# Kernel optimization log

Measured on AMD Instinct MI355X. Metric: run time of the kernel, lower is better.

The kernel has to match this reference:

```python
import jax, jax.numpy as jnp
import numpy as np

S, B, D, N, DH = 2048, 2, 1024, 16, 64  # seq, batch, d_model, n_head, d_head
LN_EPS = 1e-5


def setup_inputs() -> dict:
    key = jax.random.key(0)
    ks = jax.random.split(key, 8)
    h = jax.random.normal(ks[0], (S, B, D), dtype=jnp.float32)
    Wq = jax.random.normal(ks[1], (D, N * DH), dtype=jnp.float32) * 0.02
    Wkv = jax.random.normal(ks[2], (D, 2 * N * DH), dtype=jnp.float32) * 0.02
    Wo = jax.random.normal(ks[3], (N * DH, D), dtype=jnp.float32) * 0.02
    ln_gamma = jnp.ones((D,), dtype=jnp.float32)
    ln_beta = jnp.zeros((D,), dtype=jnp.float32)
    # persistent compressive-memory state from a previous segment
    memory = jax.random.normal(ks[4], (B, N, DH, DH), dtype=jnp.float32)
    # normalization is a sum of (elu(k)+1) over ~S positions -> strictly positive, O(S)
    mem_norm = jax.random.uniform(ks[5], (B, 1, N, DH), dtype=jnp.float32) * S + 1.0
    gate_beta = jnp.ones((1,), dtype=jnp.float32) * 0.01  # beta_eps
    return {"h": h, "Wq": Wq, "Wkv": Wkv, "Wo": Wo, "ln_gamma": ln_gamma,
            "ln_beta": ln_beta, "memory": memory, "mem_norm": mem_norm,
            "gate_beta": gate_beta}


def reference(h, Wq, Wkv, Wo, ln_gamma, ln_beta, memory, mem_norm, gate_beta):
    scale = 1.0 / np.sqrt(DH).astype(np.float32)
    # projections (pre_lnorm=False, mems=None -> c == h)
    q = (h @ Wq).reshape(S, B, N, DH)
    k, v = jnp.split(h @ Wkv, 2, axis=-1)
    k = k.reshape(S, B, N, DH)
    v = v.reshape(S, B, N, DH)
    # local quadratic attention
    score = jnp.einsum('ibnd,jbnd->ijbn', q, k) * scale  # [S,S,B,N]
    prob = jax.nn.softmax(score, axis=1)
    attn_vec = jnp.einsum('ijbn,jbnd->ibnd', prob, v).reshape(S, B, N * DH)
    # memory retrieval (NOTE: source swaps K/V in the _update_memory call;
    # it is done under no_grad -> stop_gradient here)
    cached_Q = jax.nn.elu(q.swapaxes(0, 1)) + 1.0          # [B,S,N,DH]
    num = jnp.einsum('bsnk,bnkv->bsnv', cached_Q, memory)   # [B,S,N,DH]
    den = jnp.einsum('bsnk,bvnk->bsnv', cached_Q, mem_norm)  # [B,S,N,1]
    content_A = jax.lax.stop_gradient(num / den)            # [B,S,N,DH]
    # gated injection
    g = jax.nn.sigmoid(gate_beta)                           # [1]
    inj = g * content_A.swapaxes(0, 1).reshape(S, B, N * DH) + (1.0 - g) * attn_vec
    attn_out = inj @ Wo
    # post layernorm residual
    y = h + attn_out
    mu = jnp.mean(y, axis=-1, keepdims=True)
    var = jnp.mean((y - mu) ** 2, axis=-1, keepdims=True)
    return (y - mu) / jnp.sqrt(var + LN_EPS) * ln_gamma + ln_beta
```

## Files before the change

kernel.cpp:

```cpp
#include <hip/hip_runtime.h>


typedef unsigned short ushort_t;
typedef unsigned int uint32;

typedef __bf16 bf16x8 __attribute__((ext_vector_type(8)));
typedef float f32x4 __attribute__((ext_vector_type(4)));
typedef float f32x16 __attribute__((ext_vector_type(16)));
typedef unsigned short u16x8 __attribute__((ext_vector_type(8)));
typedef unsigned short u16x4 __attribute__((ext_vector_type(4)));
typedef unsigned int u32x4 __attribute__((ext_vector_type(4)));

typedef const __attribute__((address_space(1))) void gvoid_t;
typedef __attribute__((address_space(3))) void lvoid_t;

#define S_LEN 2048
#define BATCH 2
#define NHEAD 16

__device__ __forceinline__ ushort_t f2bf(float x) {
  union { float f; unsigned u; } c; c.f = x;
  unsigned r = (c.u + 0x7FFFu + ((c.u >> 16) & 1u)) >> 16;
  return (ushort_t)r;
}
__device__ __forceinline__ float bf2f(ushort_t v) {
  union { unsigned u; float f; } c; c.u = ((unsigned)v) << 16;
  return c.f;
}

__global__ __launch_bounds__(256) void k_cvt_h(const float* __restrict__ src,
                                               ushort_t* __restrict__ dst, int n4) {
  int idx = blockIdx.x * 256 + threadIdx.x;
  if (idx >= n4) return;
  float4 v = ((const float4*)src)[idx];
  u16x4 o; o[0] = f2bf(v.x); o[1] = f2bf(v.y); o[2] = f2bf(v.z); o[3] = f2bf(v.w);
  ((u16x4*)dst)[idx] = o;
}

__global__ __launch_bounds__(256) void k_cvt_wT(const float* __restrict__ W,
                                                ushort_t* __restrict__ WT, int K, int N) {
  __shared__ float tile[32][33];
  const int n0 = blockIdx.x * 32, k0 = blockIdx.y * 32;
  const int tx = threadIdx.x & 31, ty = threadIdx.x >> 5;
#pragma unroll
  for (int r = 0; r < 32; r += 8)
    tile[ty + r][tx] = W[(size_t)(k0 + ty + r) * N + n0 + tx];
  __syncthreads();
#pragma unroll
  for (int r = 0; r < 32; r += 8)
    WT[(size_t)(n0 + ty + r) * K + k0 + tx] = f2bf(tile[tx][ty + r]);
}

template <int OUT_BF16>
__global__ __launch_bounds__(256) void k_gemm_bt(const ushort_t* __restrict__ A,
                                                 const ushort_t* __restrict__ B,
                                                 void* __restrict__ Cv, int M, int N, int K,
                                                 int nbx) {
  __shared__ __attribute__((aligned(16))) ushort_t As[128 * 32];
  __shared__ __attribute__((aligned(16))) ushort_t Bs[128 * 32];
  const int per = gridDim.x >> 3;
  const int fl = (blockIdx.x & 7) * per + (blockIdx.x >> 3);
  const int m0 = (fl / nbx) * 128, n0 = (fl % nbx) * 128;
  const int tid = threadIdx.x, w = tid >> 6, lane = tid & 63;
  const int wm = (w >> 1) * 64, wn = (w & 1) * 64;
  const int l15 = lane & 15, l4 = lane >> 4;
  f32x4 acc[4][4];
#pragma unroll
  for (int i = 0; i < 4; ++i)
#pragma unroll
    for (int j = 0; j < 4; ++j)
#pragma unroll
      for (int r = 0; r < 4; ++r) acc[i][j][r] = 0.f;

  for (int k0 = 0; k0 < K; k0 += 32) {
    __syncthreads();
#pragma unroll
    for (int r = 0; r < 2; ++r) {
      int c = r * 256 + w * 64 + lane;
      const ushort_t* ga = A + (size_t)(m0 + (c >> 2)) * K + k0 + (c & 3) * 8;
      const ushort_t* gb = B + (size_t)(n0 + (c >> 2)) * K + k0 + (c & 3) * 8;
      __builtin_amdgcn_global_load_lds((gvoid_t*)ga, (lvoid_t*)(As + (r * 256 + w * 64) * 8), 16, 0, 0);
      __builtin_amdgcn_global_load_lds((gvoid_t*)gb, (lvoid_t*)(Bs + (r * 256 + w * 64) * 8), 16, 0, 0);
    }
    __syncthreads();
    bf16x8 af[4], bfr[4];
#pragma unroll
    for (int i = 0; i < 4; ++i) af[i] = *(const bf16x8*)&As[(wm + i * 16 + l15) * 32 + l4 * 8];
#pragma unroll
    for (int j = 0; j < 4; ++j) bfr[j] = *(const bf16x8*)&Bs[(wn + j * 16 + l15) * 32 + l4 * 8];
#pragma unroll
    for (int i = 0; i < 4; ++i)
#pragma unroll
      for (int j = 0; j < 4; ++j)
        acc[i][j] = __builtin_amdgcn_mfma_f32_16x16x32_bf16(af[i], bfr[j], acc[i][j], 0, 0, 0);
  }
#pragma unroll
  for (int i = 0; i < 4; ++i)
#pragma unroll
    for (int j = 0; j < 4; ++j)
#pragma unroll
      for (int r = 0; r < 4; ++r) {
        int row = m0 + wm + i * 16 + l4 * 4 + r;
        int col = n0 + wn + j * 16 + l15;
        if (OUT_BF16)
          ((ushort_t*)Cv)[(size_t)row * N + col] = f2bf(acc[i][j][r]);
        else
          ((float*)Cv)[(size_t)row * N + col] = acc[i][j][r];
      }
}

__global__ __launch_bounds__(256) void k_gemm64(const ushort_t* __restrict__ A,
                                                const ushort_t* __restrict__ B,
                                                float* __restrict__ C, int M, int N, int K,
                                                int nbx) {
  __shared__ __attribute__((aligned(16))) ushort_t As[64 * 32];
  __shared__ __attribute__((aligned(16))) ushort_t Bs[128 * 32];
  const int per = gridDim.x >> 3;
  const int fl = (blockIdx.x & 7) * per + (blockIdx.x >> 3);
  const int m0 = (fl / nbx) * 64, n0 = (fl % nbx) * 128;
  const int tid = threadIdx.x, w = tid >> 6, lane = tid & 63;
  const int wn = w * 32;
  const int l15 = lane & 15, l4 = lane >> 4;
  f32x4 acc[4][2];
#pragma unroll
  for (int i = 0; i < 4; ++i)
#pragma unroll
    for (int j = 0; j < 2; ++j)
#pragma unroll
      for (int r = 0; r < 4; ++r) acc[i][j][r] = 0.f;

  for (int k0 = 0; k0 < K; k0 += 32) {
    __syncthreads();
    {
      int c = w * 64 + lane;
      const ushort_t* ga = A + (size_t)(m0 + (c >> 2)) * K + k0 + (c & 3) * 8;
      __builtin_amdgcn_global_load_lds((gvoid_t*)ga, (lvoid_t*)(As + w * 512), 16, 0, 0);
#pragma unroll
      for (int r = 0; r < 2; ++r) {
        int c2 = r * 256 + w * 64 + lane;
        const ushort_t* gb = B + (size_t)(n0 + (c2 >> 2)) * K + k0 + (c2 & 3) * 8;
        __builtin_amdgcn_global_load_lds((gvoid_t*)gb, (lvoid_t*)(Bs + r * 2048 + w * 512), 16, 0, 0);
      }
    }
    __syncthreads();
    bf16x8 af[4], bfr[2];
#pragma unroll
    for (int i = 0; i < 4; ++i) af[i] = *(const bf16x8*)&As[(i * 16 + l15) * 32 + l4 * 8];
#pragma unroll
    for (int j = 0; j < 2; ++j) bfr[j] = *(const bf16x8*)&Bs[(wn + j * 16 + l15) * 32 + l4 * 8];
#pragma unroll
    for (int i = 0; i < 4; ++i)
#pragma unroll
      for (int j = 0; j < 2; ++j)
        acc[i][j] = __builtin_amdgcn_mfma_f32_16x16x32_bf16(af[i], bfr[j], acc[i][j], 0, 0, 0);
  }
#pragma unroll
  for (int i = 0; i < 4; ++i)
#pragma unroll
    for (int j = 0; j < 2; ++j)
#pragma unroll
      for (int r = 0; r < 4; ++r)
        C[(size_t)(m0 + i * 16 + l4 * 4 + r) * N + n0 + wn + j * 16 + l15] = acc[i][j][r];
}

__global__ __launch_bounds__(256) void k_vt(const ushort_t* __restrict__ qkv,
                                            ushort_t* __restrict__ vt) {
  __shared__ uint32 tile[64 * 65];
  const int jt = blockIdx.x, bn = blockIdx.y, b = bn & 1, n = bn >> 1;
  const int tid = threadIdx.x;
  const int j0 = jt * 64;
#pragma unroll
  for (int rr = 0; rr < 2; ++rr) {
    int lin = rr * 2048 + tid * 8;
    int j = lin >> 6, d0 = lin & 63;
    u16x8 v = *(const u16x8*)(qkv + (size_t)(j0 + j) * 6144 + b * 3072 + 2048 + n * 64 + d0);
#pragma unroll
    for (int e = 0; e < 8; ++e) tile[j * 65 + d0 + e] = v[e];
  }
  __syncthreads();
#pragma unroll
  for (int rr = 0; rr < 2; ++rr) {
    int lin = rr * 2048 + tid * 8;
    int d = lin >> 6, jj = lin & 63;
    u16x8 o;
#pragma unroll
    for (int e = 0; e < 8; ++e) o[e] = (ushort_t)tile[(jj + e) * 65 + d];
    *(u16x8*)(vt + ((size_t)bn * 64 + d) * 2048 + j0 + jj) = o;
  }
}

__device__ __forceinline__ void stage_k(const ushort_t* __restrict__ qkv, ushort_t* kw,
                                        int j0, int b, int n, int w, int lane) {
#pragma unroll
  for (int r = 0; r < 2; ++r) {
    int jb_ = w * 16 + r * 8;
    int jb8 = w * 2 + r;
    const ushort_t* ksrc = qkv + (size_t)(j0 + jb_ + (lane >> 3)) * 6144 + b * 3072 + n * 64 + 1024
                           + ((((lane & 7) ^ (lane >> 3) ^ jb8) & 7) << 3);
    __builtin_amdgcn_global_load_lds((gvoid_t*)ksrc, (lvoid_t*)(kw + jb_ * 64), 16, 0, 0);
  }
}
__device__ __forceinline__ void stage_vt(const ushort_t* __restrict__ vt, ushort_t* vw,
                                         int j0, int bn, int w, int lane) {
#pragma unroll
  for (int r = 0; r < 2; ++r) {
    int db_ = w * 16 + r * 8;
    int jb8 = w * 2 + r;
    const ushort_t* vsrc = vt + ((size_t)bn * 64 + db_ + (lane >> 3)) * 2048 + j0
                           + ((((lane & 7) ^ (lane >> 3) ^ jb8) & 7) << 3);
    __builtin_amdgcn_global_load_lds((gvoid_t*)vsrc, (lvoid_t*)(vw + db_ * 64), 16, 0, 0);
  }
}

__global__ __launch_bounds__(256) void k_attn(const ushort_t* __restrict__ qkv,
                                              const ushort_t* __restrict__ vt,
                                              const float* __restrict__ mem,
                                              const float* __restrict__ mnorm,
                                              const float* __restrict__ gbeta,
                                              ushort_t* __restrict__ inj) {
  __shared__ __attribute__((aligned(16))) ushort_t Ks[2][4096];
  __shared__ __attribute__((aligned(16))) ushort_t VTs[2][4096];
  const int bn = blockIdx.y, b = bn & 1, n = bn >> 1;
  const int tid = threadIdx.x, w = tid >> 6, lane = tid & 63;
  const int l31 = lane & 31, h = lane >> 5;
  const int qrow = blockIdx.x * 128 + w * 32 + l31;
  const size_t qoff = (size_t)qrow * 6144 + b * 3072 + n * 64;
  const float CEXP = 0.18033688011113723f;
  bf16x8 qf[4];
#pragma unroll
  for (int ks = 0; ks < 4; ++ks) {
    u16x8 qv = *(const u16x8*)(qkv + qoff + ks * 16 + h * 8);
    union { u16x8 u; bf16x8 v; } cu;
#pragma unroll
    for (int e = 0; e < 8; ++e) cu.u[e] = f2bf(bf2f(qv[e]) * CEXP);
    qf[ks] = cu.v;
  }
  const int fA = (l31 & 7) ^ (l31 >> 3);
  const int fB = fA ^ 4;
  union { u16x8 u; bf16x8 v; } ones;
#pragma unroll
  for (int e = 0; e < 8; ++e) ones.u[e] = 0x3F80;

  stage_k(qkv, Ks[0], 0, b, n, w, lane);
  stage_vt(vt, VTs[0], 0, bn, w, lane);
  __syncthreads();

  f32x16 oacc[2], lacc;
#pragma unroll
  for (int r = 0; r < 16; ++r) { oacc[0][r] = 0.f; oacc[1][r] = 0.f; lacc[r] = 0.f; }

  for (int t = 0; t < 32; ++t) {
    const ushort_t* Kb = Ks[t & 1];
    const ushort_t* Vb = VTs[t & 1];
    if (t < 31) {
      stage_k(qkv, Ks[(t + 1) & 1], (t + 1) * 64, b, n, w, lane);
      stage_vt(vt, VTs[(t + 1) & 1], (t + 1) * 64, bn, w, lane);
    }
    f32x16 sv[2];
#pragma unroll
    for (int r = 0; r < 16; ++r) { sv[0][r] = 0.f; sv[1][r] = 0.f; }
    __builtin_amdgcn_s_setprio(1);
#pragma unroll
    for (int jb = 0; jb < 2; ++jb) {
      const int rb = (jb * 32 + l31) * 64;
      const int fj = jb ? fB : fA;
#pragma unroll
      for (int ks = 0; ks < 4; ++ks) {
        bf16x8 kf = *(const bf16x8*)&Kb[rb + ((((ks << 1) | h) ^ fj) << 3)];
        sv[jb] = __builtin_amdgcn_mfma_f32_32x32x16_bf16(kf, qf[ks], sv[jb], 0, 0, 0);
      }
    }
    __builtin_amdgcn_s_setprio(0);
#pragma unroll
    for (int jb = 0; jb < 2; ++jb)
#pragma unroll
      for (int r = 0; r < 16; ++r)
        sv[jb][r] = __builtin_amdgcn_exp2f(sv[jb][r]);
#pragma unroll
    for (int ks = 0; ks < 4; ++ks) {
      const int jb = ks >> 1, q0 = (ks & 1) * 2;
      uint32 X0, X1, Y0, Y1;
      asm volatile("v_cvt_pk_bf16_f32 %0, %1, %2" : "=v"(X0) : "v"(sv[jb][q0 * 4 + 0]), "v"(sv[jb][q0 * 4 + 1]));
      asm volatile("v_cvt_pk_bf16_f32 %0, %1, %2" : "=v"(X1) : "v"(sv[jb][q0 * 4 + 2]), "v"(sv[jb][q0 * 4 + 3]));
      asm volatile("v_cvt_pk_bf16_f32 %0, %1, %2" : "=v"(Y0) : "v"(sv[jb][(q0 + 1) * 4 + 0]), "v"(sv[jb][(q0 + 1) * 4 + 1]));
      asm volatile("v_cvt_pk_bf16_f32 %0, %1, %2" : "=v"(Y1) : "v"(sv[jb][(q0 + 1) * 4 + 2]), "v"(sv[jb][(q0 + 1) * 4 + 3]));
      asm volatile("v_permlane32_swap_b32 %0, %1" : "+v"(X0), "+v"(Y0));
      asm volatile("v_permlane32_swap_b32 %0, %1" : "+v"(X1), "+v"(Y1));
      union { u32x4 u; bf16x8 v; } pf;
      pf.u[0] = X0; pf.u[1] = X1; pf.u[2] = Y0; pf.u[3] = Y1;
      const int c = (ks << 1) | h;
      bf16x8 vf0 = *(const bf16x8*)&Vb[l31 * 64 + ((c ^ fA) << 3)];
      bf16x8 vf1 = *(const bf16x8*)&Vb[(32 + l31) * 64 + ((c ^ fB) << 3)];
      __builtin_amdgcn_s_setprio(1);
      oacc[0] = __builtin_amdgcn_mfma_f32_32x32x16_bf16(vf0, pf.v, oacc[0], 0, 0, 0);
      oacc[1] = __builtin_amdgcn_mfma_f32_32x32x16_bf16(vf1, pf.v, oacc[1], 0, 0, 0);
      lacc = __builtin_amdgcn_mfma_f32_32x32x16_bf16(ones.v, pf.v, lacc, 0, 0, 0);
      __builtin_amdgcn_s_setprio(0);
    }
    if (t < 31) __syncthreads();
  }
  const float l_run = lacc[0];

  float den = 0.f;
  bf16x8 cqf[4];
  const float* nrm = mnorm + (size_t)(b * NHEAD + n) * 64;
#pragma unroll
  for (int ks = 0; ks < 4; ++ks) {
    u16x8 qv = *(const u16x8*)(qkv + qoff + ks * 16 + h * 8);
    union { u16x8 u; bf16x8 v; } cu;
#pragma unroll
    for (int e = 0; e < 8; ++e) {
      float x = bf2f(qv[e]);
      float c = (x > 0.f) ? (x + 1.f) : __builtin_amdgcn_exp2f(x * 1.4426950408889634f);
      cu.u[e] = f2bf(c);
      den += c * nrm[ks * 16 + h * 8 + e];
    }
    cqf[ks] = cu.v;
  }
  den += __shfl_xor(den, 32);

  const float* mb = mem + (size_t)(b * NHEAD + n) * 4096;
  f32x16 accv[2];
#pragma unroll
  for (int r = 0; r < 16; ++r) { accv[0][r] = 0.f; accv[1][r] = 0.f; }
#pragma unroll
  for (int db = 0; db < 2; ++db)
#pragma unroll
    for (int ks = 0; ks < 4; ++ks) {
      union { u16x8 u; bf16x8 v; } af;
#pragma unroll
      for (int e = 0; e < 8; ++e)
        af.u[e] = f2bf(mb[(size_t)(ks * 16 + h * 8 + e) * 64 + db * 32 + l31]);
      accv[db] = __builtin_amdgcn_mfma_f32_32x32x16_bf16(af.v, cqf[ks], accv[db], 0, 0, 0);
    }

  float g = 1.f / (1.f + expf(-gbeta[0]));
  float rden = 1.f / den, invl = 1.f / l_run;
  ushort_t* op = inj + (size_t)qrow * 2048 + b * 1024 + n * 64;
#pragma unroll
  for (int db = 0; db < 2; ++db)
#pragma unroll
    for (int qq = 0; qq < 4; ++qq) {
      u16x4 st;
#pragma unroll
      for (int m = 0; m < 4; ++m) {
        float content = accv[db][qq * 4 + m] * rden;
        float av = oacc[db][qq * 4 + m] * invl;
        st[m] = f2bf(g * content + (1.f - g) * av);
      }
      *(u16x4*)(op + db * 32 + qq * 8 + h * 4) = st;
    }
}

__global__ __launch_bounds__(256) void k_ln(const float* __restrict__ h,
                                            const float* __restrict__ ao,
                                            const float* __restrict__ gam,
                                            const float* __restrict__ bet,
                                            float* __restrict__ out) {
  const int m = blockIdx.x, t = threadIdx.x;
  const int lane = t & 63, w = t >> 6;
  __shared__ float redS[4], redQ[4];
  const size_t base = (size_t)m * 1024;
  float4 hv = ((const float4*)(h + base))[t];
  float4 avv = ((const float4*)(ao + base))[t];
  float y0 = hv.x + avv.x, y1 = hv.y + avv.y, y2 = hv.z + avv.z, y3 = hv.w + avv.w;
  float s = y0 + y1 + y2 + y3;
  float sq = y0 * y0 + y1 * y1 + y2 * y2 + y3 * y3;
#pragma unroll
  for (int mk = 32; mk >= 1; mk >>= 1) { s += __shfl_xor(s, mk); sq += __shfl_xor(sq, mk); }
  if (lane == 0) { redS[w] = s; redQ[w] = sq; }
  __syncthreads();
  float Ssum = redS[0] + redS[1] + redS[2] + redS[3];
  float Qsum = redQ[0] + redQ[1] + redQ[2] + redQ[3];
  float mu = Ssum * (1.f / 1024.f);
  float var = Qsum * (1.f / 1024.f) - mu * mu;
  float rstd = rsqrtf(var + 1e-5f);
  float4 g = ((const float4*)gam)[t];
  float4 bt = ((const float4*)bet)[t];
  float4 o;
  o.x = (y0 - mu) * rstd * g.x + bt.x;
  o.y = (y1 - mu) * rstd * g.y + bt.y;
  o.z = (y2 - mu) * rstd * g.z + bt.z;
  o.w = (y3 - mu) * rstd * g.w + bt.w;
  ((float4*)(out + base))[t] = o;
}

extern "C" void kernel_launch(void* const* d_in, const int* in_sizes, int n_in,
                              void* d_out, int out_size, void* d_ws, size_t ws_size,
                              hipStream_t stream) {
  const float* h = (const float*)d_in[0];
  const float* Wq = (const float*)d_in[1];
  const float* Wkv = (const float*)d_in[2];
  const float* Wo = (const float*)d_in[3];
  const float* gam = (const float*)d_in[4];
  const float* bet = (const float*)d_in[5];
  const float* mem = (const float*)d_in[6];
  const float* mnorm = (const float*)d_in[7];
  const float* gbeta = (const float*)d_in[8];
  float* out = (float*)d_out;

  char* ws = (char*)d_ws;
  ushort_t* hb  = (ushort_t*)(ws);
  ushort_t* wT  = (ushort_t*)(ws + (size_t)(8u << 20));
  ushort_t* woT = (ushort_t*)(ws + (size_t)(14u << 20));
  ushort_t* qkv = (ushort_t*)(ws + (size_t)(16u << 20));
  float*    ao  = (float*)   (ws + (size_t)(16u << 20));
  ushort_t* vtb = (ushort_t*)(ws + (size_t)(40u << 20));
  ushort_t* inj = hb;

  k_cvt_h<<<4096, 256, 0, stream>>>(h, hb, 1048576);
  k_cvt_wT<<<dim3(32, 32), 256, 0, stream>>>(Wq, wT, 1024, 1024);
  k_cvt_wT<<<dim3(64, 32), 256, 0, stream>>>(Wkv, wT + (size_t)1024 * 1024, 1024, 2048);
  k_cvt_wT<<<dim3(32, 32), 256, 0, stream>>>(Wo, woT, 1024, 1024);
  k_gemm_bt<1><<<768, 256, 0, stream>>>(hb, wT, (void*)qkv, 4096, 3072, 1024, 24);
  k_vt<<<dim3(32, 32), 256, 0, stream>>>(qkv, vtb);
  k_attn<<<dim3(16, 32), 256, 0, stream>>>(qkv, vtb, mem, mnorm, gbeta, inj);
  k_gemm64<<<512, 256, 0, stream>>>(inj, woT, ao, 4096, 1024, 1024, 8);
  k_ln<<<4096, 256, 0, stream>>>(h, ao, gam, bet, out);
}
```

Measured before the change: 145.8 us.

## Triple-buffer attention K/V staging with vmcnt waits; merge weight conversion launches

The attention kernel moves from a double to a triple LDS buffer for K and V^T tiles. It prefetches two tiles ahead and uses explicit s_waitcnt vmcnt counts with raw barriers instead of __syncthreads, so global-to-LDS loads overlap more compute. Separately, the three weight transpose/convert launches are merged into one 3D-grid launch to cut launch overhead, with some early-exit blocks for the narrower weights. The change uses more LDS per block, which could lower occupancy, and the vmcnt counts must match the number of loads issued per stage to stay correct.

```diff
diff --git a/kernel.cpp b/kernel.cpp
--- a/kernel.cpp
+++ b/kernel.cpp
@@ -37,8 +37,20 @@
   ((u16x4*)dst)[idx] = o;
 }
 
-__global__ __launch_bounds__(256) void k_cvt_wT(const float* __restrict__ W,
-                                                ushort_t* __restrict__ WT, int K, int N) {
+__global__ __launch_bounds__(256) void k_cvt_wT3(const float* __restrict__ Wq,
+                                                 const float* __restrict__ Wkv,
+                                                 const float* __restrict__ Wo,
+                                                 ushort_t* __restrict__ wT,
+                                                 ushort_t* __restrict__ woT) {
+  const int z = blockIdx.z;
+  const float* W;
+  ushort_t* WT;
+  int N;
+  if (z == 0)      { W = Wq;  WT = wT;                          N = 1024; }
+  else if (z == 1) { W = Wkv; WT = wT + (size_t)1024 * 1024;    N = 2048; }
+  else             { W = Wo;  WT = woT;                         N = 1024; }
+  const int K = 1024;
+  if (blockIdx.x * 32 >= N) return;
   __shared__ float tile[32][33];
   const int n0 = blockIdx.x * 32, k0 = blockIdx.y * 32;
   const int tx = threadIdx.x & 31, ty = threadIdx.x >> 5;
@@ -218,8 +230,8 @@
                                               const float* __restrict__ mnorm,
                                               const float* __restrict__ gbeta,
                                               ushort_t* __restrict__ inj) {
-  __shared__ __attribute__((aligned(16))) ushort_t Ks[2][4096];
-  __shared__ __attribute__((aligned(16))) ushort_t VTs[2][4096];
+  __shared__ __attribute__((aligned(16))) ushort_t Ks[3][4096];
+  __shared__ __attribute__((aligned(16))) ushort_t VTs[3][4096];
   const int bn = blockIdx.y, b = bn & 1, n = bn >> 1;
   const int tid = threadIdx.x, w = tid >> 6, lane = tid & 63;
   const int l31 = lane & 31, h = lane >> 5;
@@ -243,19 +255,26 @@
 
   stage_k(qkv, Ks[0], 0, b, n, w, lane);
   stage_vt(vt, VTs[0], 0, bn, w, lane);
-  __syncthreads();
+  stage_k(qkv, Ks[1], 64, b, n, w, lane);
+  stage_vt(vt, VTs[1], 64, bn, w, lane);
 
   f32x16 oacc[2], lacc;
 #pragma unroll
   for (int r = 0; r < 16; ++r) { oacc[0][r] = 0.f; oacc[1][r] = 0.f; lacc[r] = 0.f; }
 
+  int cur = 0, stg = 2;
   for (int t = 0; t < 32; ++t) {
-    const ushort_t* Kb = Ks[t & 1];
-    const ushort_t* Vb = VTs[t & 1];
-    if (t < 31) {
-      stage_k(qkv, Ks[(t + 1) & 1], (t + 1) * 64, b, n, w, lane);
-      stage_vt(vt, VTs[(t + 1) & 1], (t + 1) * 64, bn, w, lane);
-    }
+    if (t + 2 < 32) {
+      stage_k(qkv, Ks[stg], (t + 2) * 64, b, n, w, lane);
+      stage_vt(vt, VTs[stg], (t + 2) * 64, bn, w, lane);
+    }
+    if (t < 30)       asm volatile("s_waitcnt vmcnt(8)" ::: "memory");
+    else if (t == 30) asm volatile("s_waitcnt vmcnt(4)" ::: "memory");
+    else              asm volatile("s_waitcnt vmcnt(0)" ::: "memory");
+    __builtin_amdgcn_s_barrier();
+
+    const ushort_t* Kb = Ks[cur];
+    const ushort_t* Vb = VTs[cur];
     f32x16 sv[2];
 #pragma unroll
     for (int r = 0; r < 16; ++r) { sv[0][r] = 0.f; sv[1][r] = 0.f; }
@@ -297,7 +316,9 @@
       lacc = __builtin_amdgcn_mfma_f32_32x32x16_bf16(ones.v, pf.v, lacc, 0, 0, 0);
       __builtin_amdgcn_s_setprio(0);
     }
-    if (t < 31) __syncthreads();
+    __builtin_amdgcn_s_barrier();
+    cur = (cur + 1 == 3) ? 0 : cur + 1;
+    stg = (stg + 1 == 3) ? 0 : stg + 1;
   }
   const float l_run = lacc[0];
 
@@ -409,9 +430,7 @@
   ushort_t* inj = hb;
 
   k_cvt_h<<<4096, 256, 0, stream>>>(h, hb, 1048576);
-  k_cvt_wT<<<dim3(32, 32), 256, 0, stream>>>(Wq, wT, 1024, 1024);
-  k_cvt_wT<<<dim3(64, 32), 256, 0, stream>>>(Wkv, wT + (size_t)1024 * 1024, 1024, 2048);
-  k_cvt_wT<<<dim3(32, 32), 256, 0, stream>>>(Wo, woT, 1024, 1024);
+  k_cvt_wT3<<<dim3(64, 32, 3), 256, 0, stream>>>(Wq, Wkv, Wo, wT, woT);
   k_gemm_bt<1><<<768, 256, 0, stream>>>(hb, wT, (void*)qkv, 4096, 3072, 1024, 24);
   k_vt<<<dim3(32, 32), 256, 0, stream>>>(qkv, vtb);
   k_attn<<<dim3(16, 32), 256, 0, stream>>>(qkv, vtb, mem, mnorm, gbeta, inj);
```

Result: no change. 145.0 us (-0.5%).
